# Performance work log

Hardware: AMD Instinct MI355X
Metric: run time of the kernel (lower is better)

The kernel has to match this reference:

```python
import jax, jax.numpy as jnp
import numpy as np

N, E, F, H, L, G, EMB, C = 50000, 600000, 128, 128, 4, 64, 64, 10
BN_EPS = 1e-5


def setup_inputs() -> dict:
    key = jax.random.key(0)
    k = lambda i: jax.random.fold_in(key, i)
    s = 0.05  # weight scale
    return {
        "x": jax.random.normal(k(0), (N, F), jnp.float32),
        "edge_index": jax.random.randint(k(1), (2, E), 0, N, jnp.int64),
        "batch": jnp.sort(jax.random.randint(k(2), (N,), 0, G, jnp.int64)),
        "emb": jax.random.normal(k(3), (G, EMB), jnp.float32),
        "eps": jnp.zeros((L,), jnp.float32),
        "W1": jax.random.normal(k(4), (L, F, H), jnp.float32) * s,
        "b1": jnp.zeros((L, H), jnp.float32),
        "W2": jax.random.normal(k(5), (L, H, H), jnp.float32) * s,
        "b2": jnp.zeros((L, H), jnp.float32),
        "gamma": jnp.ones((L, H), jnp.float32),
        "beta": jnp.zeros((L, H), jnp.float32),
        "lin1_w": jax.random.normal(k(6), (L * H + EMB, 2 * H), jnp.float32) * s,
        "lin1_b": jnp.zeros((2 * H,), jnp.float32),
        "lin2_w": jax.random.normal(k(7), (2 * H, H), jnp.float32) * s,
        "lin2_b": jnp.zeros((H,), jnp.float32),
        "lin4_w": jax.random.normal(k(8), (H, C), jnp.float32) * s,
        "lin4_b": jnp.zeros((C,), jnp.float32),
    }


def _gin_mlp(h, W1, b1, W2, b2, gamma, beta):
    # Linear -> ReLU -> Linear -> ReLU -> BatchNorm1d (batch stats)
    h = jax.nn.relu(h @ W1 + b1)
    h = jax.nn.relu(h @ W2 + b2)
    mean = jnp.mean(h, axis=0)
    var = jnp.var(h, axis=0)
    return (h - mean) * jax.lax.rsqrt(var + BN_EPS) * gamma + beta


def reference(x, edge_index, batch, emb, eps, W1, b1, W2, b2, gamma, beta,
              lin1_w, lin1_b, lin2_w, lin2_b, lin4_w, lin4_b):
    src, dst = edge_index[0], edge_index[1]
    xs = []
    for l in range(L):
        # GIN: MLP((1+eps)*x_i + sum_{j->i} x_j)  via gather + scatter-add
        agg = jax.ops.segment_sum(x[src], dst, num_segments=N)  # [N,H]
        x = _gin_mlp((1.0 + eps[l]) * x + agg,
                     W1[l], b1[l], W2[l], b2[l], gamma[l], beta[l])
        xs.append(x)
    h = jnp.concatenate(xs, axis=1)  # [N, L*H]
    # global mean pool per graph
    sums = jax.ops.segment_sum(h, batch, num_segments=G)  # [G, L*H]
    cnt = jax.ops.segment_sum(jnp.ones((N,), h.dtype), batch, num_segments=G)
    pooled = sums / jnp.maximum(cnt, 1.0)[:, None]
    z = jnp.concatenate([pooled, emb.reshape(G, -1)], axis=1)
    z = jax.nn.relu(z @ lin1_w + lin1_b)  # .relu() twice is idempotent
    # dropout p=0.5 skipped (eval mode); lin3 unused in original forward
    z = jax.nn.relu(z @ lin2_w + lin2_b)
    z = z @ lin4_w + lin4_b
    return jax.nn.log_softmax(z, axis=1)
```

## Files before the change

### kernel.cpp

```cpp
#include <hip/hip_runtime.h>
#include <cstdint>
#include <cstddef>

#define N_NODES 50000
#define N_EDGES 600000
#define NLAYER  4
#define NGRAPH  64
#define SCAN_NB 196
#define NBLK_MLP ((N_NODES + 127) / 128)
#define RED_B    ((NBLK_MLP + 12) / 13)

typedef unsigned int   u32;
typedef unsigned short u16;
typedef unsigned char  u8;
typedef float f32x4  __attribute__((ext_vector_type(4)));
typedef short bf16x8 __attribute__((ext_vector_type(8)));

__device__ __forceinline__ float bf1(u16 u)  { return __uint_as_float(((u32)u) << 16); }
__device__ __forceinline__ float bflo(u32 u) { return __uint_as_float(u << 16); }
__device__ __forceinline__ float bfhi(u32 u) { return __uint_as_float(u & 0xffff0000u); }
__device__ __forceinline__ u16 f2bf(float f) {
    u32 x = __float_as_uint(f);
    u32 r = x + 0x7fffu + ((x >> 16) & 1u);
    return (u16)(r >> 16);
}
__device__ __forceinline__ u32 pack2(float a, float b) {
    return (u32)f2bf(a) | ((u32)f2bf(b) << 16);
}

__device__ __forceinline__ float fp8b0(u32 u) { return __builtin_amdgcn_cvt_f32_fp8(u, 0); }
__device__ __forceinline__ float fp8b1(u32 u) { return __builtin_amdgcn_cvt_f32_fp8(u, 1); }
__device__ __forceinline__ u32 pk_fp8(float a, float b) {
    return (u32)__builtin_amdgcn_cvt_pk_fp8_f32(a, b, 0, false);
}

__global__ __launch_bounds__(256) void cvt_x(const float4* __restrict__ x,
                                             u32* __restrict__ xf8) {
    int i = blockIdx.x * 256 + threadIdx.x;
    if (i < N_NODES * 32) {
        float4 v = x[i];
        u32 r = pk_fp8(v.x, v.y);
        r = (u32)__builtin_amdgcn_cvt_pk_fp8_f32(v.z, v.w, (int)r, true);
        xf8[i] = r;
    }
}

__global__ __launch_bounds__(128) void cvt_w(const float* __restrict__ W1,
                                             const float* __restrict__ W2,
                                             short* __restrict__ W1t,
                                             short* __restrict__ W2t) {
    int l = blockIdx.y, n = blockIdx.x, k = threadIdx.x;
    const float* W = blockIdx.z ? W2 : W1;
    short* Wt      = blockIdx.z ? W2t : W1t;
    Wt[((size_t)l * 128 + n) * 128 + k] = (short)f2bf(W[((size_t)l * 128 + k) * 128 + n]);
}

__global__ void count_deg(const int* __restrict__ dst, int* __restrict__ deg) {
    int e = blockIdx.x * 256 + threadIdx.x;
    if (e < N_EDGES) atomicAdd(&deg[dst[e]], 1);
}

__global__ __launch_bounds__(256) void scan_l1(const int* __restrict__ deg,
                                               int* __restrict__ bscan,
                                               int* __restrict__ bsum) {
    __shared__ int sd[256];
    int tid = threadIdx.x;
    int i = blockIdx.x * 256 + tid;
    int v = (i < N_NODES) ? deg[i] : 0;
    sd[tid] = v; __syncthreads();
#pragma unroll
    for (int off = 1; off < 256; off <<= 1) {
        int t = (tid >= off) ? sd[tid - off] : 0;
        __syncthreads();
        sd[tid] += t; __syncthreads();
    }
    if (i < N_NODES) bscan[i] = sd[tid];
    if (tid == 255) bsum[blockIdx.x] = sd[255];
}

__global__ __launch_bounds__(256) void scan_l2(const int* __restrict__ bsum,
                                               int* __restrict__ boff) {
    __shared__ int sd[256];
    int tid = threadIdx.x;
    int v = (tid < SCAN_NB) ? bsum[tid] : 0;
    sd[tid] = v; __syncthreads();
#pragma unroll
    for (int off = 1; off < 256; off <<= 1) {
        int t = (tid >= off) ? sd[tid - off] : 0;
        __syncthreads();
        sd[tid] += t; __syncthreads();
    }
    if (tid < SCAN_NB) boff[tid] = sd[tid] - v;
}

__global__ __launch_bounds__(256) void scan_l3(const int* __restrict__ bscan,
                                               const int* __restrict__ boff,
                                               int* __restrict__ rowp) {
    int i = blockIdx.x * 256 + threadIdx.x;
    if (i == 0) rowp[0] = 0;
    if (i < N_NODES) rowp[i + 1] = bscan[i] + boff[blockIdx.x];
}

__global__ void fill_csr(const int* __restrict__ src, const int* __restrict__ dst,
                         const int* __restrict__ rowp, int* __restrict__ cursor,
                         int* __restrict__ col) {
    int e = blockIdx.x * 256 + threadIdx.x;
    if (e < N_EDGES) {
        int d = dst[e];
        int pos = atomicAdd(&cursor[d], 1);
        col[rowp[d] + pos] = src[e];
    }
}

__global__ __launch_bounds__(256) void agg_kernel(
    const u16* __restrict__ xin,
    const float* __restrict__ coef,
    const int* __restrict__ rowp, const int* __restrict__ col,
    const float* __restrict__ eps_all, int layer,
    u32* __restrict__ agg) {
    int node = blockIdx.x * 4 + (threadIdx.x >> 6);
    int lane = threadIdx.x & 63;
    if (node >= N_NODES) return;
    float a0 = 1.f, a1 = 1.f, d0 = 0.f, d1 = 0.f;
    if (coef) {
        a0 = coef[2 * lane];       a1 = coef[2 * lane + 1];
        d0 = coef[128 + 2 * lane]; d1 = coef[128 + 2 * lane + 1];
    }
    float ep = 1.0f + eps_all[layer];
    u32 v = xin[(size_t)node * 64 + lane];
    int k0 = rowp[node], k1 = rowp[node + 1];
    float s0 = 0.f, s1 = 0.f;
    int k = k0;
    int cc[8];
    if (k < k1) {
#pragma unroll
        for (int t = 0; t < 8; t++) cc[t] = col[min(k + t, k1 - 1)];
    }
    while (k < k1) {
        int idx[8];
#pragma unroll
        for (int t = 0; t < 8; t++) idx[t] = cc[t];
        int kn = k + 8;
        if (kn < k1) {
#pragma unroll
            for (int t = 0; t < 8; t++) cc[t] = col[min(kn + t, k1 - 1)];
        }
#pragma unroll
        for (int t = 0; t < 8; t++) {
            u32 u = xin[(size_t)idx[t] * 64 + lane];
            float w = (k + t < k1) ? 1.f : 0.f;
            s0 += w * fp8b0(u); s1 += w * fp8b1(u);
        }
        k = kn;
    }
    float deg = (float)(k1 - k0);
    float r0 = ep * (a0 * fp8b0(v) + d0) + a0 * s0 + deg * d0;
    float r1 = ep * (a1 * fp8b1(v) + d1) + a1 * s1 + deg * d1;
    agg[(size_t)node * 64 + lane] = pack2(r0, r1);
}

#define H1_STRIDE 136
__global__ __launch_bounds__(256) void mlp_fused(
    const short* __restrict__ A,
    const short* __restrict__ W1t, const float* __restrict__ b1,
    const short* __restrict__ W2t, const float* __restrict__ b2,
    u8* __restrict__ H2, const int* __restrict__ batch,
    float* __restrict__ partial, float* __restrict__ gsum, int M) {
    __shared__ alignas(16) short h1s[128 * H1_STRIDE];
    __shared__ int sh_ga, sh_gb, sh_split;
    int tid  = threadIdx.x;
    int wave = tid >> 6, lane = tid & 63;
    int ln15 = lane & 15, quad = lane >> 4;
    int m0blk = blockIdx.x * 128;
    int m0 = m0blk + wave * 32;
    const bf16x8 zz = {0, 0, 0, 0, 0, 0, 0, 0};

    if (tid == 0) {
        int rlo = m0blk, rhi = min(m0blk + 127, M - 1);
        int ga = batch[rlo], gb = batch[rhi];
        int split = m0blk + 128;
        if (ga != gb) {
            int lo = rlo, hi = rhi;
            while (lo + 1 < hi) { int mid = (lo + hi) >> 1; if (batch[mid] == ga) lo = mid; else hi = mid; }
            split = hi;
        }
        sh_ga = ga; sh_gb = gb; sh_split = split;
    }

    bf16x8 a[2][4];
#pragma unroll
    for (int rt = 0; rt < 2; rt++) {
        int row = m0 + rt * 16 + ln15;
        const short* rp = A + (size_t)row * 128 + quad * 8;
        bool ok = row < M;
#pragma unroll
        for (int s = 0; s < 4; s++)
            a[rt][s] = ok ? *(const bf16x8*)(rp + s * 32) : zz;
    }
#pragma unroll
    for (int ct = 0; ct < 8; ct++) {
        const short* wp = W1t + (size_t)(ct * 16 + ln15) * 128 + quad * 8;
        bf16x8 b[4];
#pragma unroll
        for (int s = 0; s < 4; s++) b[s] = *(const bf16x8*)(wp + s * 32);
        float bias = b1[ct * 16 + ln15];
#pragma unroll
        for (int rt = 0; rt < 2; rt++) {
            f32x4 acc = {0.f, 0.f, 0.f, 0.f};
#pragma unroll
            for (int s = 0; s < 4; s++)
                acc = __builtin_amdgcn_mfma_f32_16x16x32_bf16(a[rt][s], b[s], acc, 0, 0, 0);
#pragma unroll
            for (int i = 0; i < 4; i++) {
                float v = fmaxf(acc[i] + bias, 0.f);
                int lr = wave * 32 + rt * 16 + quad * 4 + i;
                h1s[lr * H1_STRIDE + ct * 16 + ln15] = (short)f2bf(v);
            }
        }
    }
    __syncthreads();
    bf16x8 c[2][4];
#pragma unroll
    for (int rt = 0; rt < 2; rt++) {
        const short* rp = h1s + (size_t)(wave * 32 + rt * 16 + ln15) * H1_STRIDE + quad * 8;
#pragma unroll
        for (int s = 0; s < 4; s++) c[rt][s] = *(const bf16x8*)(rp + s * 32);
    }
    int gsplit = sh_split;
    float sAcc[8], qAcc[8], pAcc[8];
#pragma unroll
    for (int ct = 0; ct < 8; ct++) { sAcc[ct] = 0.f; qAcc[ct] = 0.f; pAcc[ct] = 0.f; }
#pragma unroll
    for (int ct = 0; ct < 8; ct++) {
        const short* wp = W2t + (size_t)(ct * 16 + ln15) * 128 + quad * 8;
        bf16x8 b[4];
#pragma unroll
        for (int s = 0; s < 4; s++) b[s] = *(const bf16x8*)(wp + s * 32);
        float bias = b2[ct * 16 + ln15];
#pragma unroll
        for (int rt = 0; rt < 2; rt++) {
            f32x4 acc = {0.f, 0.f, 0.f, 0.f};
#pragma unroll
            for (int s = 0; s < 4; s++)
                acc = __builtin_amdgcn_mfma_f32_16x16x32_bf16(c[rt][s], b[s], acc, 0, 0, 0);
            int colx = ct * 16 + ln15;
#pragma unroll
            for (int i = 0; i < 4; i++) {
                int row = m0 + rt * 16 + quad * 4 + i;
                float v = fmaxf(acc[i] + bias, 0.f);
                if (row < M) H2[(size_t)row * 128 + colx] = (u8)(pk_fp8(v, v) & 0xffu);
                float vm = (row < M) ? v : 0.f;
                sAcc[ct] += vm; qAcc[ct] += vm * vm;
                if (row < gsplit) pAcc[ct] += vm;
            }
        }
    }
    __syncthreads();
    float* scr = (float*)h1s;
    int slice = wave * 4 + quad;
#pragma unroll
    for (int ct = 0; ct < 8; ct++) {
        int colx = ct * 16 + ln15;
        scr[(0 * 16 + slice) * 128 + colx] = sAcc[ct];
        scr[(1 * 16 + slice) * 128 + colx] = qAcc[ct];
        scr[(2 * 16 + slice) * 128 + colx] = pAcc[ct];
    }
    __syncthreads();
    if (tid < 128) {
        float ss = 0.f, qq = 0.f, pa = 0.f;
#pragma unroll
        for (int sl = 0; sl < 16; sl++) {
            ss += scr[(0 * 16 + sl) * 128 + tid];
            qq += scr[(1 * 16 + sl) * 128 + tid];
            pa += scr[(2 * 16 + sl) * 128 + tid];
        }
        partial[(size_t)blockIdx.x * 256 + tid]       = ss;
        partial[(size_t)blockIdx.x * 256 + 128 + tid] = qq;
        int ga = sh_ga, gb = sh_gb;
        atomicAdd(&gsum[ga * 128 + tid], pa);
        if (gb != ga) atomicAdd(&gsum[gb * 128 + tid], ss - pa);
    }
}

__global__ __launch_bounds__(256) void reduce_finalize(
    const float* __restrict__ partial, float* __restrict__ sums,
    int* __restrict__ red_cnt,
    const float* __restrict__ gamma, const float* __restrict__ beta,
    int layer, float* __restrict__ coef) {
    int t = threadIdx.x;
    int b0 = blockIdx.x * 13, b1 = min(b0 + 13, NBLK_MLP);
    if (b0 < NBLK_MLP) {
        float acc = 0.f;
        for (int b = b0; b < b1; b++) acc += partial[(size_t)b * 256 + t];
        atomicAdd(&sums[t], acc);
    }
    __threadfence();
    __shared__ int is_last;
    if (t == 0) is_last = (atomicAdd(red_cnt, 1) == gridDim.x - 1) ? 1 : 0;
    __syncthreads();
    if (is_last && t < 128) {
        float s1 = atomicAdd(&sums[t], 0.f);
        float s2 = atomicAdd(&sums[128 + t], 0.f);
        float mean = s1 / (float)N_NODES;
        float var  = s2 / (float)N_NODES - mean * mean;
        float istd = rsqrtf(var + 1e-5f);
        float a = istd * gamma[layer * 128 + t];
        coef[t]       = a;
        coef[128 + t] = beta[layer * 128 + t] - mean * a;
    }
}

__global__ __launch_bounds__(256) void head_kernel(
    const float* __restrict__ gsum, const float* __restrict__ coefL,
    const int* __restrict__ batch, const float* __restrict__ emb,
    const float* __restrict__ l1w, const float* __restrict__ l1b,
    const float* __restrict__ l2w, const float* __restrict__ l2b,
    const float* __restrict__ l4w, const float* __restrict__ l4b,
    float* __restrict__ out) {
    __shared__ float z[576];
    __shared__ float z1[256];
    __shared__ float z2h[2][128];
    __shared__ float z2[128];
    __shared__ float zr[128][10];
    __shared__ float inv_cnt;
    int g = blockIdx.x;
    int tid = threadIdx.x;
    if (tid == 0) {
        int lo = 0, hi = N_NODES;
        while (lo < hi) { int m = (lo + hi) >> 1; if (batch[m] < g) lo = m + 1; else hi = m; }
        int s = lo;
        lo = 0; hi = N_NODES;
        while (lo < hi) { int m = (lo + hi) >> 1; if (batch[m] < g + 1) lo = m + 1; else hi = m; }
        inv_cnt = 1.0f / fmaxf((float)(lo - s), 1.0f);
    }
    __syncthreads();
    for (int j = tid; j < 512; j += 256) {
        int l = j >> 7, c = j & 127;
        float a = coefL[l * 256 + c], d = coefL[l * 256 + 128 + c];
        z[j] = a * gsum[(size_t)l * NGRAPH * 128 + g * 128 + c] * inv_cnt + d;
    }
    if (tid < 64) z[512 + tid] = emb[g * 64 + tid];
    __syncthreads();
    {
        float acc = l1b[tid];
        for (int j0 = 0; j0 < 576; j0 += 16) {
            float lw[16];
#pragma unroll
            for (int t = 0; t < 16; t++) lw[t] = l1w[(j0 + t) * 256 + tid];
#pragma unroll
            for (int t = 0; t < 16; t++) acc += z[j0 + t] * lw[t];
        }
        z1[tid] = fmaxf(acc, 0.f);
    }
    __syncthreads();
    {
        int c2 = tid & 127, half = tid >> 7;
        float acc = 0.f;
        int jb = half * 128;
        for (int j0 = 0; j0 < 128; j0 += 8) {
            float lw[8];
#pragma unroll
            for (int t = 0; t < 8; t++) lw[t] = l2w[(jb + j0 + t) * 128 + c2];
#pragma unroll
            for (int t = 0; t < 8; t++) acc += z1[jb + j0 + t] * lw[t];
        }
        z2h[half][c2] = acc;
    }
    __syncthreads();
    if (tid < 128) z2[tid] = fmaxf(z2h[0][tid] + z2h[1][tid] + l2b[tid], 0.f);
    __syncthreads();
    if (tid < 128) {
        float zv = z2[tid];
        const float* wr = l4w + tid * 10;
#pragma unroll
        for (int c = 0; c < 10; c++) zr[tid][c] = zv * wr[c];
    }
    __syncthreads();
    for (int s = 64; s >= 1; s >>= 1) {
        if (tid < s) {
#pragma unroll
            for (int c = 0; c < 10; c++) zr[tid][c] += zr[tid + s][c];
        }
        __syncthreads();
    }
    if (tid == 0) {
        float z3s[10];
#pragma unroll
        for (int c = 0; c < 10; c++) z3s[c] = zr[0][c] + l4b[c];
        float m = z3s[0];
        for (int i = 1; i < 10; i++) m = fmaxf(m, z3s[i]);
        float se = 0.f;
        for (int i = 0; i < 10; i++) se += expf(z3s[i] - m);
        float lse = m + logf(se);
        for (int i = 0; i < 10; i++) out[g * 10 + i] = z3s[i] - lse;
    }
}

extern "C" void kernel_launch(void* const* d_in, const int* in_sizes, int n_in,
                              void* d_out, int out_size, void* d_ws, size_t ws_size,
                              hipStream_t stream) {
    (void)in_sizes; (void)n_in; (void)out_size; (void)ws_size;
    const float* x0   = (const float*)d_in[0];
    const int* ei     = (const int*)d_in[1];
    const int* src    = ei;
    const int* dst    = ei + N_EDGES;
    const int* batch  = (const int*)d_in[2];
    const float* emb  = (const float*)d_in[3];
    const float* eps  = (const float*)d_in[4];
    const float* W1   = (const float*)d_in[5];
    const float* b1   = (const float*)d_in[6];
    const float* W2   = (const float*)d_in[7];
    const float* b2   = (const float*)d_in[8];
    const float* gamma= (const float*)d_in[9];
    const float* beta = (const float*)d_in[10];
    const float* l1w  = (const float*)d_in[11];
    const float* l1b  = (const float*)d_in[12];
    const float* l2w  = (const float*)d_in[13];
    const float* l2b  = (const float*)d_in[14];
    const float* l4w  = (const float*)d_in[15];
    const float* l4b  = (const float*)d_in[16];

    char* ws = (char*)d_ws;
    size_t off = 0;
    auto alloc = [&](size_t bytes) -> char* {
        char* p = ws + off; off += (bytes + 255) & ~(size_t)255; return p;
    };
    int* deg    = (int*)alloc(N_NODES * 4);
    int* cursor = (int*)alloc(N_NODES * 4);
    int* red_cnt = (int*)alloc(NLAYER * 4);
    float* sumsL = (float*)alloc(NLAYER * 256 * 4);
    float* gsumL = (float*)alloc((size_t)NLAYER * NGRAPH * 128 * 4);
    size_t zero_len = (char*)gsumL - (char*)deg + (size_t)NLAYER * NGRAPH * 128 * 4;
    int* rowp   = (int*)alloc((N_NODES + 1) * 4);
    int* bscan  = (int*)alloc(N_NODES * 4);
    int* bsum   = (int*)alloc(SCAN_NB * 4);
    int* boff   = (int*)alloc(SCAN_NB * 4);
    int* col    = (int*)alloc(N_EDGES * 4);
    u8* xf8     = (u8*)alloc((size_t)N_NODES * 128);
    u8* h2a     = (u8*)alloc((size_t)N_NODES * 128);
    u8* h2b     = (u8*)alloc((size_t)N_NODES * 128);
    u32* agg    = (u32*)alloc((size_t)N_NODES * 64 * 4);
    short* W1t  = (short*)alloc((size_t)NLAYER * 128 * 128 * 2);
    short* W2t  = (short*)alloc((size_t)NLAYER * 128 * 128 * 2);
    float* partial = (float*)alloc((size_t)NBLK_MLP * 256 * 4);
    float* coefL = (float*)alloc(NLAYER * 256 * 4);

    hipMemsetAsync(deg, 0, zero_len, stream);

    cvt_x<<<(N_NODES * 32 + 255) / 256, 256, 0, stream>>>((const float4*)x0, (u32*)xf8);
    {
        dim3 gw(128, NLAYER, 2);
        cvt_w<<<gw, 128, 0, stream>>>(W1, W2, W1t, W2t);
    }
    count_deg<<<(N_EDGES + 255) / 256, 256, 0, stream>>>(dst, deg);
    scan_l1<<<SCAN_NB, 256, 0, stream>>>(deg, bscan, bsum);
    scan_l2<<<1, 256, 0, stream>>>(bsum, boff);
    scan_l3<<<SCAN_NB, 256, 0, stream>>>(bscan, boff, rowp);
    fill_csr<<<(N_EDGES + 255) / 256, 256, 0, stream>>>(src, dst, rowp, cursor, col);

    const u8* xin = xf8;
    for (int l = 0; l < NLAYER; ++l) {
        u8* h2 = (l & 1) ? h2b : h2a;
        const float* coef_prev = (l == 0) ? nullptr : (coefL + (l - 1) * 256);
        agg_kernel<<<(N_NODES + 3) / 4, 256, 0, stream>>>(
            (const u16*)xin, coef_prev, rowp, col, eps, l, agg);
        mlp_fused<<<NBLK_MLP, 256, 0, stream>>>(
            (const short*)agg, W1t + (size_t)l * 16384, b1 + l * 128,
            W2t + (size_t)l * 16384, b2 + l * 128, h2, batch,
            partial, gsumL + (size_t)l * NGRAPH * 128, N_NODES);
        reduce_finalize<<<RED_B, 256, 0, stream>>>(
            partial, sumsL + l * 256, red_cnt + l, gamma, beta, l,
            coefL + l * 256);
        xin = h2;
    }
    head_kernel<<<NGRAPH, 256, 0, stream>>>(gsumL, coefL, batch, emb,
                                            l1w, l1b, l2w, l2b, l4w, l4b,
                                            (float*)d_out);
}
```

Before: 408.4 us.

## Restructure aggregation gather, fold BN finalize into consumers, merge scan kernels

The aggregation kernel now has each lane load 8 fp8 channels per neighbor, and four lane groups each handle a different neighbor. Partial sums are combined with cross-lane shuffles, which widens memory accesses and doubles the edges in flight. The separate reduce_finalize kernel is removed: the MLP kernel atomically adds its BN statistics directly, and the agg and head kernels recompute the per-channel scale and shift from those sums. The scan_l2 and scan_l3 kernels are merged so that every block redundantly scans the block sums. Together these cut launches and use wider loads, at the cost of more global atomics, redundant BN math per node, and shuffle work.

New measurement: 446.2 us. 1.09x slower.

```diff
diff --git a/kernel.cpp b/kernel.cpp
--- a/kernel.cpp
+++ b/kernel.cpp
@@ -8,17 +8,15 @@
 #define NGRAPH  64
 #define SCAN_NB 196
 #define NBLK_MLP ((N_NODES + 127) / 128)
-#define RED_B    ((NBLK_MLP + 12) / 13)
 
 typedef unsigned int   u32;
 typedef unsigned short u16;
 typedef unsigned char  u8;
 typedef float f32x4  __attribute__((ext_vector_type(4)));
 typedef short bf16x8 __attribute__((ext_vector_type(8)));
-
-__device__ __forceinline__ float bf1(u16 u)  { return __uint_as_float(((u32)u) << 16); }
-__device__ __forceinline__ float bflo(u32 u) { return __uint_as_float(u << 16); }
-__device__ __forceinline__ float bfhi(u32 u) { return __uint_as_float(u & 0xffff0000u); }
+typedef u32 u32x2 __attribute__((ext_vector_type(2)));
+typedef u32 u32x4 __attribute__((ext_vector_type(4)));
+
 __device__ __forceinline__ u16 f2bf(float f) {
     u32 x = __float_as_uint(f);
     u32 r = x + 0x7fffu + ((x >> 16) & 1u);
@@ -28,10 +26,16 @@
     return (u32)f2bf(a) | ((u32)f2bf(b) << 16);
 }
 
-__device__ __forceinline__ float fp8b0(u32 u) { return __builtin_amdgcn_cvt_f32_fp8(u, 0); }
-__device__ __forceinline__ float fp8b1(u32 u) { return __builtin_amdgcn_cvt_f32_fp8(u, 1); }
 __device__ __forceinline__ u32 pk_fp8(float a, float b) {
     return (u32)__builtin_amdgcn_cvt_pk_fp8_f32(a, b, 0, false);
+}
+__device__ __forceinline__ float fp8b(u32 u, int j) {
+    switch (j) {
+    case 0:  return __builtin_amdgcn_cvt_f32_fp8(u, 0);
+    case 1:  return __builtin_amdgcn_cvt_f32_fp8(u, 1);
+    case 2:  return __builtin_amdgcn_cvt_f32_fp8(u, 2);
+    default: return __builtin_amdgcn_cvt_f32_fp8(u, 3);
+    }
 }
 
 __global__ __launch_bounds__(256) void cvt_x(const float4* __restrict__ x,
@@ -78,9 +82,11 @@
     if (tid == 255) bsum[blockIdx.x] = sd[255];
 }
 
-__global__ __launch_bounds__(256) void scan_l2(const int* __restrict__ bsum,
-                                               int* __restrict__ boff) {
+__global__ __launch_bounds__(256) void scan_l3(const int* __restrict__ bscan,
+                                               const int* __restrict__ bsum,
+                                               int* __restrict__ rowp) {
     __shared__ int sd[256];
+    __shared__ int sboff;
     int tid = threadIdx.x;
     int v = (tid < SCAN_NB) ? bsum[tid] : 0;
     sd[tid] = v; __syncthreads();
@@ -90,15 +96,11 @@
         __syncthreads();
         sd[tid] += t; __syncthreads();
     }
-    if (tid < SCAN_NB) boff[tid] = sd[tid] - v;
-}
-
-__global__ __launch_bounds__(256) void scan_l3(const int* __restrict__ bscan,
-                                               const int* __restrict__ boff,
-                                               int* __restrict__ rowp) {
-    int i = blockIdx.x * 256 + threadIdx.x;
+    if (tid == (int)blockIdx.x) sboff = sd[tid] - v;
+    __syncthreads();
+    int i = blockIdx.x * 256 + tid;
     if (i == 0) rowp[0] = 0;
-    if (i < N_NODES) rowp[i + 1] = bscan[i] + boff[blockIdx.x];
+    if (i < N_NODES) rowp[i + 1] = bscan[i] + sboff;
 }
 
 __global__ void fill_csr(const int* __restrict__ src, const int* __restrict__ dst,
@@ -113,50 +115,104 @@
 }
 
 __global__ __launch_bounds__(256) void agg_kernel(
-    const u16* __restrict__ xin,
-    const float* __restrict__ coef,
+    const u8* __restrict__ xin,
+    const float* __restrict__ sums,
+    const float* __restrict__ gamma, const float* __restrict__ beta,
     const int* __restrict__ rowp, const int* __restrict__ col,
     const float* __restrict__ eps_all, int layer,
     u32* __restrict__ agg) {
     int node = blockIdx.x * 4 + (threadIdx.x >> 6);
     int lane = threadIdx.x & 63;
     if (node >= N_NODES) return;
-    float a0 = 1.f, a1 = 1.f, d0 = 0.f, d1 = 0.f;
-    if (coef) {
-        a0 = coef[2 * lane];       a1 = coef[2 * lane + 1];
-        d0 = coef[128 + 2 * lane]; d1 = coef[128 + 2 * lane + 1];
+    int g  = lane >> 4;
+    int ch = lane & 15;
+
+    float A[8], D[8];
+    if (sums) {
+        int lc = (layer - 1) * 128 + ch * 8;
+#pragma unroll
+        for (int j = 0; j < 8; j++) {
+            int c = ch * 8 + j;
+            float s1 = sums[c], s2 = sums[128 + c];
+            float mean = s1 * (1.0f / N_NODES);
+            float var  = s2 * (1.0f / N_NODES) - mean * mean;
+            float a = rsqrtf(var + 1e-5f) * gamma[lc + j];
+            A[j] = a;
+            D[j] = beta[lc + j] - mean * a;
+        }
+    } else {
+#pragma unroll
+        for (int j = 0; j < 8; j++) { A[j] = 1.f; D[j] = 0.f; }
     }
     float ep = 1.0f + eps_all[layer];
-    u32 v = xin[(size_t)node * 64 + lane];
     int k0 = rowp[node], k1 = rowp[node + 1];
-    float s0 = 0.f, s1 = 0.f;
+    float s[8];
+#pragma unroll
+    for (int j = 0; j < 8; j++) s[j] = 0.f;
+
+    const u8* rowbase = xin + ch * 8;
+    int cc[4]; u32x2 rr[4];
     int k = k0;
-    int cc[8];
     if (k < k1) {
 #pragma unroll
-        for (int t = 0; t < 8; t++) cc[t] = col[min(k + t, k1 - 1)];
+        for (int t = 0; t < 4; t++) cc[t] = col[min(k + t * 4 + g, k1 - 1)];
+#pragma unroll
+        for (int t = 0; t < 4; t++) rr[t] = *(const u32x2*)(rowbase + (size_t)cc[t] * 128);
     }
     while (k < k1) {
-        int idx[8];
-#pragma unroll
-        for (int t = 0; t < 8; t++) idx[t] = cc[t];
-        int kn = k + 8;
-        if (kn < k1) {
-#pragma unroll
-            for (int t = 0; t < 8; t++) cc[t] = col[min(kn + t, k1 - 1)];
-        }
-#pragma unroll
-        for (int t = 0; t < 8; t++) {
-            u32 u = xin[(size_t)idx[t] * 64 + lane];
-            float w = (k + t < k1) ? 1.f : 0.f;
-            s0 += w * fp8b0(u); s1 += w * fp8b1(u);
+        int kn = k + 16;
+        bool more = kn < k1;
+        int c2[4];
+        if (more) {
+#pragma unroll
+            for (int t = 0; t < 4; t++) c2[t] = col[min(kn + t * 4 + g, k1 - 1)];
+        }
+        u32 u[8];
+#pragma unroll
+        for (int t = 0; t < 4; t++) {
+            bool ok = (k + t * 4 + g) < k1;
+            u[2 * t]     = ok ? rr[t].x : 0u;
+            u[2 * t + 1] = ok ? rr[t].y : 0u;
+        }
+        if (more) {
+#pragma unroll
+            for (int t = 0; t < 4; t++) rr[t] = *(const u32x2*)(rowbase + (size_t)c2[t] * 128);
+#pragma unroll
+            for (int t = 0; t < 4; t++) cc[t] = c2[t];
+        }
+#pragma unroll
+        for (int t = 0; t < 4; t++) {
+#pragma unroll
+            for (int j = 0; j < 4; j++) {
+                s[j]     += fp8b(u[2 * t],     j);
+                s[4 + j] += fp8b(u[2 * t + 1], j);
+            }
         }
         k = kn;
     }
+#pragma unroll
+    for (int j = 0; j < 8; j++) {
+        s[j] += __shfl_xor(s[j], 16);
+        s[j] += __shfl_xor(s[j], 32);
+    }
+    u32x2 sv = *(const u32x2*)(rowbase + (size_t)node * 128);
     float deg = (float)(k1 - k0);
-    float r0 = ep * (a0 * fp8b0(v) + d0) + a0 * s0 + deg * d0;
-    float r1 = ep * (a1 * fp8b1(v) + d1) + a1 * s1 + deg * d1;
-    agg[(size_t)node * 64 + lane] = pack2(r0, r1);
+    float r[8];
+#pragma unroll
+    for (int j = 0; j < 4; j++) {
+        float x0 = fp8b(sv.x, j);
+        float x1 = fp8b(sv.y, j);
+        r[j]     = ep * (A[j]     * x0 + D[j])     + A[j]     * s[j]     + deg * D[j];
+        r[4 + j] = ep * (A[4 + j] * x1 + D[4 + j]) + A[4 + j] * s[4 + j] + deg * D[4 + j];
+    }
+    if (g == 0) {
+        u32x4 o;
+        o.x = pack2(r[0], r[1]);
+        o.y = pack2(r[2], r[3]);
+        o.z = pack2(r[4], r[5]);
+        o.w = pack2(r[6], r[7]);
+        *(u32x4*)(agg + (size_t)node * 64 + ch * 4) = o;
+    }
 }
 
 #define H1_STRIDE 136
@@ -165,7 +221,7 @@
     const short* __restrict__ W1t, const float* __restrict__ b1,
     const short* __restrict__ W2t, const float* __restrict__ b2,
     u8* __restrict__ H2, const int* __restrict__ batch,
-    float* __restrict__ partial, float* __restrict__ gsum, int M) {
+    float* __restrict__ sums, float* __restrict__ gsum, int M) {
     __shared__ alignas(16) short h1s[128 * H1_STRIDE];
     __shared__ int sh_ga, sh_gb, sh_split;
     int tid  = threadIdx.x;
@@ -274,44 +330,17 @@
             qq += scr[(1 * 16 + sl) * 128 + tid];
             pa += scr[(2 * 16 + sl) * 128 + tid];
         }
-        partial[(size_t)blockIdx.x * 256 + tid]       = ss;
-        partial[(size_t)blockIdx.x * 256 + 128 + tid] = qq;
+        atomicAdd(&sums[tid], ss);
+        atomicAdd(&sums[128 + tid], qq);
         int ga = sh_ga, gb = sh_gb;
         atomicAdd(&gsum[ga * 128 + tid], pa);
         if (gb != ga) atomicAdd(&gsum[gb * 128 + tid], ss - pa);
     }
 }
 
-__global__ __launch_bounds__(256) void reduce_finalize(
-    const float* __restrict__ partial, float* __restrict__ sums,
-    int* __restrict__ red_cnt,
+__global__ __launch_bounds__(256) void head_kernel(
+    const float* __restrict__ gsum, const float* __restrict__ sumsL,
     const float* __restrict__ gamma, const float* __restrict__ beta,
-    int layer, float* __restrict__ coef) {
-    int t = threadIdx.x;
-    int b0 = blockIdx.x * 13, b1 = min(b0 + 13, NBLK_MLP);
-    if (b0 < NBLK_MLP) {
-        float acc = 0.f;
-        for (int b = b0; b < b1; b++) acc += partial[(size_t)b * 256 + t];
-        atomicAdd(&sums[t], acc);
-    }
-    __threadfence();
-    __shared__ int is_last;
-    if (t == 0) is_last = (atomicAdd(red_cnt, 1) == gridDim.x - 1) ? 1 : 0;
-    __syncthreads();
-    if (is_last && t < 128) {
-        float s1 = atomicAdd(&sums[t], 0.f);
-        float s2 = atomicAdd(&sums[128 + t], 0.f);
-        float mean = s1 / (float)N_NODES;
-        float var  = s2 / (float)N_NODES - mean * mean;
-        float istd = rsqrtf(var + 1e-5f);
-        float a = istd * gamma[layer * 128 + t];
-        coef[t]       = a;
-        coef[128 + t] = beta[layer * 128 + t] - mean * a;
-    }
-}
-
-__global__ __launch_bounds__(256) void head_kernel(
-    const float* __restrict__ gsum, const float* __restrict__ coefL,
     const int* __restrict__ batch, const float* __restrict__ emb,
     const float* __restrict__ l1w, const float* __restrict__ l1b,
     const float* __restrict__ l2w, const float* __restrict__ l2b,
@@ -336,7 +365,11 @@
     __syncthreads();
     for (int j = tid; j < 512; j += 256) {
         int l = j >> 7, c = j & 127;
-        float a = coefL[l * 256 + c], d = coefL[l * 256 + 128 + c];
+        float s1 = sumsL[l * 256 + c], s2 = sumsL[l * 256 + 128 + c];
+        float mean = s1 * (1.0f / N_NODES);
+        float var  = s2 * (1.0f / N_NODES) - mean * mean;
+        float a = rsqrtf(var + 1e-5f) * gamma[l * 128 + c];
+        float d = beta[l * 128 + c] - mean * a;
         z[j] = a * gsum[(size_t)l * NGRAPH * 128 + g * 128 + c] * inv_cnt + d;
     }
     if (tid < 64) z[512 + tid] = emb[g * 64 + tid];
@@ -427,14 +460,12 @@
     };
     int* deg    = (int*)alloc(N_NODES * 4);
     int* cursor = (int*)alloc(N_NODES * 4);
-    int* red_cnt = (int*)alloc(NLAYER * 4);
     float* sumsL = (float*)alloc(NLAYER * 256 * 4);
     float* gsumL = (float*)alloc((size_t)NLAYER * NGRAPH * 128 * 4);
     size_t zero_len = (char*)gsumL - (char*)deg + (size_t)NLAYER * NGRAPH * 128 * 4;
     int* rowp   = (int*)alloc((N_NODES + 1) * 4);
     int* bscan  = (int*)alloc(N_NODES * 4);
     int* bsum   = (int*)alloc(SCAN_NB * 4);
-    int* boff   = (int*)alloc(SCAN_NB * 4);
     int* col    = (int*)alloc(N_EDGES * 4);
     u8* xf8     = (u8*)alloc((size_t)N_NODES * 128);
     u8* h2a     = (u8*)alloc((size_t)N_NODES * 128);
@@ -442,8 +473,6 @@
     u32* agg    = (u32*)alloc((size_t)N_NODES * 64 * 4);
     short* W1t  = (short*)alloc((size_t)NLAYER * 128 * 128 * 2);
     short* W2t  = (short*)alloc((size_t)NLAYER * 128 * 128 * 2);
-    float* partial = (float*)alloc((size_t)NBLK_MLP * 256 * 4);
-    float* coefL = (float*)alloc(NLAYER * 256 * 4);
 
     hipMemsetAsync(deg, 0, zero_len, stream);
 
@@ -454,26 +483,22 @@
     }
     count_deg<<<(N_EDGES + 255) / 256, 256, 0, stream>>>(dst, deg);
     scan_l1<<<SCAN_NB, 256, 0, stream>>>(deg, bscan, bsum);
-    scan_l2<<<1, 256, 0, stream>>>(bsum, boff);
-    scan_l3<<<SCAN_NB, 256, 0, stream>>>(bscan, boff, rowp);
+    scan_l3<<<SCAN_NB, 256, 0, stream>>>(bscan, bsum, rowp);
     fill_csr<<<(N_EDGES + 255) / 256, 256, 0, stream>>>(src, dst, rowp, cursor, col);
 
     const u8* xin = xf8;
     for (int l = 0; l < NLAYER; ++l) {
         u8* h2 = (l & 1) ? h2b : h2a;
-        const float* coef_prev = (l == 0) ? nullptr : (coefL + (l - 1) * 256);
+        const float* sums_prev = (l == 0) ? nullptr : (sumsL + (l - 1) * 256);
         agg_kernel<<<(N_NODES + 3) / 4, 256, 0, stream>>>(
-            (const u16*)xin, coef_prev, rowp, col, eps, l, agg);
+            xin, sums_prev, gamma, beta, rowp, col, eps, l, agg);
         mlp_fused<<<NBLK_MLP, 256, 0, stream>>>(
             (const short*)agg, W1t + (size_t)l * 16384, b1 + l * 128,
             W2t + (size_t)l * 16384, b2 + l * 128, h2, batch,
-            partial, gsumL + (size_t)l * NGRAPH * 128, N_NODES);
-        reduce_finalize<<<RED_B, 256, 0, stream>>>(
-            partial, sumsL + l * 256, red_cnt + l, gamma, beta, l,
-            coefL + l * 256);
+            sumsL + l * 256, gsumL + (size_t)l * NGRAPH * 128, N_NODES);
         xin = h2;
     }
-    head_kernel<<<NGRAPH, 256, 0, stream>>>(gsumL, coefL, batch, emb,
+    head_kernel<<<NGRAPH, 256, 0, stream>>>(gsumL, sumsL, gamma, beta, batch, emb,
                                             l1w, l1b, l2w, l2b, l4w, l4b,
                                             (float*)d_out);
 }
```
